# Performance work log

Hardware: AMD Instinct MI355X
Metric: run time of the kernel (lower is better)

## Reference

```python
import jax, jax.numpy as jnp
import numpy as np
import math

B, L, DM = 2, 2048, 1536
H, FD = 12, 16          # num_heads, feature_dim
DV = DM // H            # head_dim = 128
D2 = FD * FD            # expanded Taylor feature dim = 256
CHUNK = 128
EPS = 1e-12
LN_EPS = 1e-5


def setup_inputs() -> dict:
    key = jax.random.key(0)
    ks = jax.random.split(key, 5)
    s = lambda fan_in: 1.0 / math.sqrt(fan_in)
    return {
        "hidden_states": jax.random.normal(ks[0], (B, L, DM), jnp.float32),
        "Wq": jax.random.normal(ks[1], (DM, H * FD), jnp.float32) * s(DM),
        "Wk": jax.random.normal(ks[2], (DM, H * FD), jnp.float32) * s(DM),
        "Wv": jax.random.normal(ks[3], (DM, H * DV), jnp.float32) * s(DM),
        "Wo": jax.random.normal(ks[4], (H * DV, DM), jnp.float32) * s(H * DV),
        "ln_q_g": jnp.ones((H * FD,), jnp.float32),
        "ln_q_b": jnp.zeros((H * FD,), jnp.float32),
        "ln_k_g": jnp.ones((H * FD,), jnp.float32),
        "ln_k_b": jnp.zeros((H * FD,), jnp.float32),
    }


def _layernorm(x, g, b):
    mu = x.mean(-1, keepdims=True)
    var = ((x - mu) ** 2).mean(-1, keepdims=True)
    return (x - mu) * jax.lax.rsqrt(var + LN_EPS) * g + b


def _taylor_exp(x):
    # x: (b, h, l, d) -> flattened outer product / sqrt(d): (b, h, l, d*d)
    x2 = x[..., :, None] * x[..., None, :]
    return x2.reshape(*x.shape[:-1], -1) / math.sqrt(FD)


def _rebased_forward(hidden_states, Wq, Wk, Wv, Wo, ln_q_g, ln_q_b, ln_k_g, ln_k_b):
    b, l, _ = hidden_states.shape
    q = _layernorm(hidden_states @ Wq, ln_q_g, ln_q_b)
    k = _layernorm(hidden_states @ Wk, ln_k_g, ln_k_b)
    v = hidden_states @ Wv
    # (b, l, h*d) -> (b, h, l, d)
    q = q.reshape(b, l, H, FD).transpose(0, 2, 1, 3)
    k = k.reshape(b, l, H, FD).transpose(0, 2, 1, 3)
    v = v.reshape(b, l, H, DV).transpose(0, 2, 1, 3)
    q2 = _taylor_exp(q)  # (b, h, l, D2)
    k2 = _taylor_exp(k)

    nC = l // CHUNK
    # chunk-major layout for scan: (nC, b, h, C, .)
    q2c = q2.reshape(b, H, nC, CHUNK, D2).transpose(2, 0, 1, 3, 4)
    k2c = k2.reshape(b, H, nC, CHUNK, D2).transpose(2, 0, 1, 3, 4)
    vc = v.reshape(b, H, nC, CHUNK, DV).transpose(2, 0, 1, 3, 4)
    mask = jnp.tril(jnp.ones((CHUNK, CHUNK), q2.dtype))  # causal within chunk

    S0 = jnp.zeros((b, H, D2, DV), q2.dtype)  # running sum of k2^T v
    z0 = jnp.zeros((b, H, D2), q2.dtype)      # running sum of k2

    def step(carry, inp):
        S, z = carry
        qc, kc, vcur = inp
        A = jnp.einsum("bhcd,bhed->bhce", qc, kc) * mask  # intra-chunk scores
        num = jnp.einsum("bhcd,bhdv->bhcv", qc, S) + jnp.einsum("bhce,bhev->bhcv", A, vcur)
        den = jnp.einsum("bhcd,bhd->bhc", qc, z) + A.sum(-1)
        o = num / (den[..., None] + EPS)
        S = S + jnp.einsum("bhed,bhev->bhdv", kc, vcur)
        z = z + kc.sum(2)
        return (S, z), o

    _, o = jax.lax.scan(step, (S0, z0), (q2c, k2c, vc))
    # (nC, b, h, C, dv) -> (b, l, h*dv)
    o = o.transpose(1, 2, 0, 3, 4).reshape(b, H, l, DV).transpose(0, 2, 1, 3).reshape(b, l, H * DV)
    return o @ Wo


def reference(hidden_states, Wq, Wk, Wv, Wo, ln_q_g, ln_q_b, ln_k_g, ln_k_b):
    return _rebased_forward(hidden_states, Wq, Wk, Wv, Wo, ln_q_g, ln_q_b, ln_k_g, ln_k_b)
```

## Files before the change

### kernel.cpp

```cpp
#include <hip/hip_runtime.h>
#include <hip/hip_bf16.h>
#include <math.h>

#define Bc   2
#define Lc   2048
#define DMc  1536
#define Hc   12
#define FDc  16
#define DVc  128
#define D2c  256
#define CHK  128
#define NCH  16
#define ROWS (Bc*Lc)
#define HFD  (Hc*FDc)
#define HDV  (Hc*DVc)
#define NQK  (2*HFD)
#define NPRJ (NQK + HDV)

typedef __bf16 bf16x8 __attribute__((ext_vector_type(8)));
typedef float f32x4 __attribute__((ext_vector_type(4)));

__device__ __forceinline__ float bf2f(unsigned short u) {
    return __uint_as_float(((unsigned int)u) << 16);
}
__device__ __forceinline__ unsigned short f2bf(float v) {
    unsigned int u = __float_as_uint(v);
    unsigned int r = (u + 0x7FFFu + ((u >> 16) & 1u)) >> 16;
    return (unsigned short)r;
}
__device__ __forceinline__ unsigned int pack2(unsigned short a, unsigned short b) {
    return (unsigned int)a | ((unsigned int)b << 16);
}
__device__ __forceinline__ float ldin(const void* p, size_t i, int isf32) {
    return isf32 ? ((const float*)p)[i] : bf2f(((const unsigned short*)p)[i]);
}

#define GLL16(g, l) __builtin_amdgcn_global_load_lds( \
    (const __attribute__((address_space(1))) unsigned int*)(g), \
    (__attribute__((address_space(3))) unsigned int*)(l), 16, 0, 0)

__global__ void probe_dtype(const unsigned short* __restrict__ hs, int* __restrict__ flag) {
    const int tid = threadIdx.x;
    int sane = 0;
    for (int i = tid; i < 1024; i += 256) {
        unsigned short b = hs[2 * i];
        int e = (b >> 7) & 0xFF;
        if (e >= 97 && e <= 157) sane++;
    }
    __shared__ int tot;
    if (tid == 0) tot = 0;
    __syncthreads();
    atomicAdd(&tot, sane);
    __syncthreads();
    if (tid == 0) *flag = (tot >= 614) ? 0 : 1;
}

__global__ __launch_bounds__(256) void prep_all(const void* __restrict__ hs,
                                                const void* __restrict__ Wq,
                                                const void* __restrict__ Wk,
                                                const void* __restrict__ Wv,
                                                const void* __restrict__ Wo,
                                                unsigned short* __restrict__ hsb,
                                                unsigned short* __restrict__ Wqkvt,
                                                unsigned short* __restrict__ Wot,
                                                const int* __restrict__ flagp) {
    const int f = *flagp;
    const int t = threadIdx.x;
    int id = blockIdx.x;
    if (id >= 1296) {
        const int n4 = ROWS * DMc / 4;
        int i = (id - 1296) * 256 + t;
        if (i < n4) {
            if (f) {
                float4 x = ((const float4*)hs)[i];
                ushort4 y;
                y.x = f2bf(x.x); y.y = f2bf(x.y); y.z = f2bf(x.z); y.w = f2bf(x.w);
                ((ushort4*)hsb)[i] = y;
            } else {
                ((ushort4*)hsb)[i] = ((const ushort4*)hs)[i];
            }
        }
        return;
    }
    __shared__ float tile[64][65];
    const void* W; unsigned short* Wt; int rows, cols, bx, by;
    if (id < 72)       { W = Wq; Wt = Wqkvt;                          rows = DMc; cols = HFD; bx = (id % 3) * 64;  by = (id / 3) * 64; }
    else if (id < 144) { id -= 72;  W = Wk; Wt = Wqkvt + (size_t)HFD * DMc; rows = DMc; cols = HFD; bx = (id % 3) * 64;  by = (id / 3) * 64; }
    else if (id < 720) { id -= 144; W = Wv; Wt = Wqkvt + (size_t)NQK * DMc; rows = DMc; cols = HDV; bx = (id % 24) * 64; by = (id / 24) * 64; }
    else               { id -= 720; W = Wo; Wt = Wot;                 rows = HDV; cols = DMc; bx = (id % 24) * 64; by = (id / 24) * 64; }
#pragma unroll
    for (int u = 0; u < 16; u++) {
        int idx = t + u * 256;
        int r = idx >> 6, c = idx & 63;
        tile[r][c] = ldin(W, (size_t)(by + r) * cols + bx + c, f);
    }
    __syncthreads();
#pragma unroll
    for (int u = 0; u < 16; u++) {
        int idx = t + u * 256;
        int r = idx >> 6, c = idx & 63;
        Wt[(size_t)(bx + r) * rows + by + c] = f2bf(tile[c][r]);
    }
}

__global__ __launch_bounds__(512) void gemm_mfma_bt(const unsigned short* __restrict__ A,
                                                    const unsigned short* __restrict__ Bt,
                                                    void* __restrict__ C,
                                                    int M, int N, int K,
                                                    int ldc,
                                                    int cMode, const int* __restrict__ flagp,
                                                    unsigned short* __restrict__ vTout) {
    const int f = *flagp;
    __shared__ __align__(16) unsigned char smem[32768];
    unsigned short* As = (unsigned short*)smem;
    unsigned short* Bsu = As + 8192;
    f32x4* scr4 = (f32x4*)smem;

    const int tid = threadIdx.x;
    const int wave = tid >> 6, lane = tid & 63;
    const int kgrp = wave >> 2;
    const int w4 = wave & 3;
    const int lin = blockIdx.y * gridDim.x + blockIdx.x;
    const int nwg = gridDim.x * gridDim.y;
    const int swz = (lin & 7) * (nwg >> 3) + (lin >> 3);
    const int row0 = (swz / gridDim.x) * 128, col0 = (swz % gridDim.x) * 128;
    const int wrow = (w4 >> 1) * 64, wcol = (w4 & 1) * 64;
    const int mlane = lane & 15, quad = lane >> 4;
    const int kHalf = K >> 1;

    const unsigned short* Ab = A + (size_t)row0 * K + (size_t)kgrp * kHalf;
    const unsigned short* Bb = Bt + (size_t)col0 * K + (size_t)kgrp * kHalf;
    const int t256 = tid & 255;
    const int r0 = t256 >> 2;
    const int kc = (t256 & 3) * 8;
    const size_t off0 = (size_t)r0 * K + kc;
    const size_t off1 = (size_t)(r0 + 64) * K + kc;
    char* AsW = (char*)As + kgrp * 8192 + w4 * 1024;
    char* BsW = (char*)Bsu + kgrp * 8192 + w4 * 1024;
    const int ldsBase = kgrp * 4096;

    f32x4 acc[4][4] = {};

    for (int k0 = 0; k0 < kHalf; k0 += 32) {
        GLL16(Ab + off0 + k0, AsW);
        GLL16(Ab + off1 + k0, AsW + 4096);
        GLL16(Bb + off0 + k0, BsW);
        GLL16(Bb + off1 + k0, BsW + 4096);
        __syncthreads();
        bf16x8 a[4], b[4];
#pragma unroll
        for (int i = 0; i < 4; i++)
            a[i] = *(const bf16x8*)&As[ldsBase + (wrow + i * 16 + mlane) * 32 + quad * 8];
#pragma unroll
        for (int j = 0; j < 4; j++)
            b[j] = *(const bf16x8*)&Bsu[ldsBase + (wcol + j * 16 + mlane) * 32 + quad * 8];
#pragma unroll
        for (int i = 0; i < 4; i++)
#pragma unroll
            for (int j = 0; j < 4; j++)
                acc[i][j] = __builtin_amdgcn_mfma_f32_16x16x32_bf16(a[i], b[j], acc[i][j], 0, 0, 0);
        __syncthreads();
    }

    {
        const int col = (wave & 1) * 64 + lane;
        if (kgrp == 1 && w4 < 2) {
#pragma unroll
            for (int i = 0; i < 4; i++)
#pragma unroll
                for (int j = 0; j < 4; j++)
                    scr4[(i * 4 + j) * 128 + col] = acc[i][j];
        }
        __syncthreads();
        if (kgrp == 0 && w4 < 2) {
#pragma unroll
            for (int i = 0; i < 4; i++)
#pragma unroll
                for (int j = 0; j < 4; j++)
                    acc[i][j] += scr4[(i * 4 + j) * 128 + col];
        }
        __syncthreads();
        if (kgrp == 1 && w4 >= 2) {
#pragma unroll
            for (int i = 0; i < 4; i++)
#pragma unroll
                for (int j = 0; j < 4; j++)
                    scr4[(i * 4 + j) * 128 + col] = acc[i][j];
        }
        __syncthreads();
        if (kgrp == 0 && w4 >= 2) {
#pragma unroll
            for (int i = 0; i < 4; i++)
#pragma unroll
                for (int j = 0; j < 4; j++)
                    acc[i][j] += scr4[(i * 4 + j) * 128 + col];
        }
    }
    if (kgrp != 0) return;

    float* Cf = nullptr;
    unsigned short* Cb16 = nullptr;
    bool doT = false;
    int tOff = 0;
    if (cMode == 0) Cf = (float*)C;
    else if (cMode == 1) Cb16 = (unsigned short*)C;
    else if (cMode == 2) { if (f) Cf = (float*)C; else Cb16 = (unsigned short*)C; }
    else if (cMode == 4) {
        if (col0 < NQK) Cf = (float*)C;
        else { doT = true; tOff = NQK; }
    }
    if (cMode <= 3 && vTout) doT = true;

#pragma unroll
    for (int i = 0; i < 4; i++)
#pragma unroll
        for (int j = 0; j < 4; j++) {
            const int col = col0 + wcol + j * 16 + mlane;
            if (Cf) {
#pragma unroll
                for (int r = 0; r < 4; r++) {
                    const int row = row0 + wrow + i * 16 + quad * 4 + r;
                    Cf[(size_t)row * ldc + col] = acc[i][j][r];
                }
            } else if (Cb16) {
#pragma unroll
                for (int r = 0; r < 4; r++) {
                    const int row = row0 + wrow + i * 16 + quad * 4 + r;
                    Cb16[(size_t)row * ldc + col] = f2bf(acc[i][j][r]);
                }
            }
            if (doT) {
                ushort4 pk;
                pk.x = f2bf(acc[i][j][0]); pk.y = f2bf(acc[i][j][1]);
                pk.z = f2bf(acc[i][j][2]); pk.w = f2bf(acc[i][j][3]);
                *(ushort4*)(vTout + (size_t)(col - tOff) * M + row0 + wrow + i * 16 + quad * 4) = pk;
            }
        }
}

__global__ __launch_bounds__(192) void ln_kernel(const float* __restrict__ qk,
                                                 float* __restrict__ q, float* __restrict__ k,
                                                 const void* __restrict__ gq,
                                                 const void* __restrict__ bq,
                                                 const void* __restrict__ gk,
                                                 const void* __restrict__ bk,
                                                 const int* __restrict__ flagp) {
    const int f = *flagp;
    const int row = blockIdx.x, t = threadIdx.x;
    float vq = qk[(size_t)row * NQK + t];
    float vk = qk[(size_t)row * NQK + HFD + t];
    float s[4] = {vq, vq * vq, vk, vk * vk};
    __shared__ float part[4][3];
    const int w = t >> 6, lane = t & 63;
#pragma unroll
    for (int i = 0; i < 4; i++) {
        float v = s[i];
        for (int off = 32; off; off >>= 1) v += __shfl_down(v, off);
        if (lane == 0) part[i][w] = v;
    }
    __syncthreads();
    float sq  = part[0][0] + part[0][1] + part[0][2];
    float sq2 = part[1][0] + part[1][1] + part[1][2];
    float sk  = part[2][0] + part[2][1] + part[2][2];
    float sk2 = part[3][0] + part[3][1] + part[3][2];
    const float inv = 1.0f / (float)HFD;
    float muq = sq * inv, muk = sk * inv;
    float varq = sq2 * inv - muq * muq;
    float vark = sk2 * inv - muk * muk;
    float oq = (vq - muq) * rsqrtf(varq + 1e-5f) * ldin(gq, t, f) + ldin(bq, t, f);
    float ok = (vk - muk) * rsqrtf(vark + 1e-5f) * ldin(gk, t, f) + ldin(bk, t, f);
    q[(size_t)row * HFD + t] = oq;
    k[(size_t)row * HFD + t] = ok;
}

__global__ __launch_bounds__(256) void state_prefix_mfma(const float* __restrict__ kn,
                                                         const unsigned short* __restrict__ vT,
                                                         unsigned short* __restrict__ St,
                                                         float* __restrict__ zc) {
    const int lin = blockIdx.x;
    const int swz = (lin & 7) * 96 + (lin >> 3);
    const int bx = swz & 15;
    const int by = (swz >> 4) & 1;
    const int bh = swz >> 5;
    const int h = bh % Hc, b = bh / Hc;
    const int t0 = bx * 16;
    const int tid = threadIdx.x;
    const int wave = tid >> 6, lane = tid & 63;
    const int mlane = lane & 15, quad = lane >> 4;

    __shared__ __align__(16) float kcs[CHK * FDc];
    __shared__ __align__(16) unsigned short K2t[16 * 136];
    __shared__ __align__(16) unsigned short Vs[64 * 136];
    __shared__ float zp[16][17];
    __shared__ float zpre[16];
    if (tid < 16) zpre[tid] = 0.f;

    f32x4 acc = {};
    const int kr = tid >> 1, khf = tid & 1;
    const int d2l = tid & 15, cg = tid >> 4;
    const int vrow = tid >> 2, vseg = tid & 3;
    const int dvL = wave * 16 + mlane;

    for (int n = 0; n < NCH; n++) {
        const int row0 = b * Lc + n * CHK;
        __syncthreads();
        {
            const float4* src = (const float4*)(kn + (size_t)(row0 + kr) * HFD + h * FDc + khf * 8);
            *(float4*)(kcs + kr * 16 + khf * 8)     = src[0];
            *(float4*)(kcs + kr * 16 + khf * 8 + 4) = src[1];
            const uint4* g = (const uint4*)(vT + (size_t)(h * 128 + by * 64 + vrow) * ROWS + row0 + vseg * 32);
            *(uint4*)(Vs + vrow * 136 + vseg * 32)      = g[0];
            *(uint4*)(Vs + vrow * 136 + vseg * 32 + 8)  = g[1];
            *(uint4*)(Vs + vrow * 136 + vseg * 32 + 16) = g[2];
            *(uint4*)(Vs + vrow * 136 + vseg * 32 + 24) = g[3];
        }
        __syncthreads();
        {
            float zs_ = 0.f;
            unsigned short pk[8];
#pragma unroll
            for (int u = 0; u < 8; u++) {
                int c = cg * 8 + u;
                float p = kcs[c * 16 + bx] * kcs[c * 16 + d2l] * 0.25f;
                zs_ += p;
                pk[u] = f2bf(p);
            }
            uint4 w;
            w.x = pack2(pk[0], pk[1]); w.y = pack2(pk[2], pk[3]);
            w.z = pack2(pk[4], pk[5]); w.w = pack2(pk[6], pk[7]);
            *(uint4*)(K2t + d2l * 136 + cg * 8) = w;
            zp[d2l][cg] = zs_;
        }
        __syncthreads();
        {
            size_t base = (((size_t)(bh * NCH + n) * 16 + bx) * 128) * 16;
            int dv = by * 64 + dvL;
            ushort4 pk;
            pk.x = f2bf(acc[0]); pk.y = f2bf(acc[1]);
            pk.z = f2bf(acc[2]); pk.w = f2bf(acc[3]);
            *(ushort4*)(St + base + (size_t)dv * 16 + quad * 4) = pk;
            if (tid < 16) {
                float s = 0.f;
#pragma unroll
                for (int c = 0; c < 16; c++) s += zp[tid][c];
                if (by == 0)
                    zc[(size_t)(bh * NCH + n) * D2c + t0 + tid] = zpre[tid];
                zpre[tid] += s;
            }
        }
        {
#pragma unroll
            for (int ks = 0; ks < 4; ks++) {
                bf16x8 a = *(const bf16x8*)(K2t + mlane * 136 + ks * 32 + quad * 8);
                bf16x8 bfr = *(const bf16x8*)(Vs + dvL * 136 + ks * 32 + quad * 8);
                acc = __builtin_amdgcn_mfma_f32_16x16x32_bf16(a, bfr, acc, 0, 0, 0);
            }
        }
    }
}

__global__ __launch_bounds__(256) void chunk_out_mfma(const float* __restrict__ qn,
                                                      const float* __restrict__ kn,
                                                      const unsigned short* __restrict__ St,
                                                      const float* __restrict__ z,
                                                      const unsigned short* __restrict__ vT,
                                                      unsigned short* __restrict__ o) {
    const int lin = blockIdx.x;
    const int blk = (lin & 7) * 48 + (lin >> 3);
    const int n = blk & 15, bh = blk >> 4;
    const int h = bh % Hc, b = bh / Hc;
    const int row0 = b * Lc + n * CHK;
    const int tid = threadIdx.x;
    const int wave = tid >> 6, lane = tid & 63;
    const int mlane = lane & 15, quad = lane >> 4;
    const int wrow = (wave >> 1) * 64, wcol = (wave & 1) * 64;

    __shared__ __align__(16) unsigned char lds[61952];
    float* Qs   = (float*)lds;
    float* zs   = (float*)(lds + 8192);
    float* denp = (float*)(lds + 9216);
    float* dinv = (float*)(lds + 10240);
    unsigned char* U = lds + 10752;
    unsigned short* Q2s = (unsigned short*)U;
    unsigned short* Sts = (unsigned short*)(U + 10240);
    unsigned short* Kb  = (unsigned short*)U;
    unsigned short* Qb  = (unsigned short*)(U + 8192);
    unsigned short* At  = (unsigned short*)(U + 16384);
    unsigned short* Vs  = (unsigned short*)U;

    {
        int r = tid >> 1, hf = tid & 1;
        const float4* src = (const float4*)(qn + (size_t)(row0 + r) * HFD + h * FDc + hf * 8);
        *(float4*)(Qs + r * 16 + hf * 8)     = src[0];
        *(float4*)(Qs + r * 16 + hf * 8 + 4) = src[1];
        if (tid < 64)
            ((float4*)zs)[tid] = ((const float4*)(z + ((size_t)bh * NCH + n) * D2c))[tid];
    }
    __syncthreads();

    const int qc = tid >> 1, qhalf = tid & 1;
    float qr[16];
#pragma unroll
    for (int ff = 0; ff < 16; ff++) qr[ff] = Qs[qc * 16 + ff];

    f32x4 acc[4][4] = {};
    float den1 = 0.f;
    const unsigned short* Stb = St + ((size_t)bh * NCH + n) * ((size_t)D2c * DVc);

    for (int k0 = 0; k0 < 256; k0 += 32) {
        {
            unsigned short pk[16];
#pragma unroll
            for (int kk = 0; kk < 16; kk++) {
                int d2 = k0 + qhalf * 16 + kk;
                float val = qr[d2 >> 4] * qr[d2 & 15] * 0.25f;
                den1 += val * zs[d2];
                pk[kk] = f2bf(val);
            }
            uint4 w0, w1;
            w0.x = pack2(pk[0], pk[1]);  w0.y = pack2(pk[2], pk[3]);
            w0.z = pack2(pk[4], pk[5]);  w0.w = pack2(pk[6], pk[7]);
            w1.x = pack2(pk[8], pk[9]);  w1.y = pack2(pk[10], pk[11]);
            w1.z = pack2(pk[12], pk[13]); w1.w = pack2(pk[14], pk[15]);
            *(uint4*)(Q2s + qc * 40 + qhalf * 16) = w0;
            *(uint4*)(Q2s + qc * 40 + qhalf * 16 + 8) = w1;
        }
        {
            int r = tid >> 1, hf = tid & 1;
            const uint4* g = (const uint4*)(Stb + (size_t)((k0 >> 4) + hf) * 2048 + r * 16);
            uint4 d0 = g[0], d1 = g[1];
            *(uint4*)(Sts + r * 40 + hf * 16) = d0;
            *(uint4*)(Sts + r * 40 + hf * 16 + 8) = d1;
        }
        __syncthreads();
        bf16x8 a[4], bfr[4];
#pragma unroll
        for (int i = 0; i < 4; i++)
            a[i] = *(const bf16x8*)(Q2s + (wrow + i * 16 + mlane) * 40 + quad * 8);
#pragma unroll
        for (int j = 0; j < 4; j++)
            bfr[j] = *(const bf16x8*)(Sts + (wcol + j * 16 + mlane) * 40 + quad * 8);
#pragma unroll
        for (int i = 0; i < 4; i++)
#pragma unroll
            for (int j = 0; j < 4; j++)
                acc[i][j] = __builtin_amdgcn_mfma_f32_16x16x32_bf16(a[i], bfr[j], acc[i][j], 0, 0, 0);
        __syncthreads();
    }
    denp[qhalf * 128 + qc] = den1;

    {
        int r = tid >> 1, hf = tid & 1;
        if (hf == 0) {
            unsigned short pq[16], pkk[16];
#pragma unroll
            for (int ff = 0; ff < 16; ff++) pq[ff] = f2bf(Qs[r * 16 + ff]);
            const float* kg = kn + (size_t)(row0 + r) * HFD + h * FDc;
#pragma unroll
            for (int ff = 0; ff < 16; ff++) pkk[ff] = f2bf(kg[ff]);
            uint4 w;
            w.x = pack2(pq[0], pq[1]);  w.y = pack2(pq[2], pq[3]);
            w.z = pack2(pq[4], pq[5]);  w.w = pack2(pq[6], pq[7]);
            *(uint4*)(Qb + r * 32) = w;
            w.x = pack2(pq[8], pq[9]);  w.y = pack2(pq[10], pq[11]);
            w.z = pack2(pq[12], pq[13]); w.w = pack2(pq[14], pq[15]);
            *(uint4*)(Qb + r * 32 + 8) = w;
            w.x = pack2(pkk[0], pkk[1]);  w.y = pack2(pkk[2], pkk[3]);
            w.z = pack2(pkk[4], pkk[5]);  w.w = pack2(pkk[6], pkk[7]);
            *(uint4*)(Kb + r * 32) = w;
            w.x = pack2(pkk[8], pkk[9]);  w.y = pack2(pkk[10], pkk[11]);
            w.z = pack2(pkk[12], pkk[13]); w.w = pack2(pkk[14], pkk[15]);
            *(uint4*)(Kb + r * 32 + 8) = w;
        } else {
            uint4 zz = make_uint4(0, 0, 0, 0);
            *(uint4*)(Qb + r * 32 + 16) = zz;
            *(uint4*)(Qb + r * 32 + 24) = zz;
            *(uint4*)(Kb + r * 32 + 16) = zz;
            *(uint4*)(Kb + r * 32 + 24) = zz;
        }
    }
    __syncthreads();

    {
        f32x4 pacc[4][4] = {};
        bf16x8 a[4], bfr[4];
#pragma unroll
        for (int i = 0; i < 4; i++)
            a[i] = *(const bf16x8*)(Qb + (wrow + i * 16 + mlane) * 32 + quad * 8);
#pragma unroll
        for (int j = 0; j < 4; j++)
            bfr[j] = *(const bf16x8*)(Kb + (wcol + j * 16 + mlane) * 32 + quad * 8);
#pragma unroll
        for (int i = 0; i < 4; i++)
#pragma unroll
            for (int j = 0; j < 4; j++)
                pacc[i][j] = __builtin_amdgcn_mfma_f32_16x16x32_bf16(a[i], bfr[j], pacc[i][j], 0, 0, 0);
#pragma unroll
        for (int i = 0; i < 4; i++)
#pragma unroll
            for (int j = 0; j < 4; j++) {
                int e = wcol + j * 16 + mlane;
#pragma unroll
                for (int r = 0; r < 4; r++) {
                    int c = wrow + i * 16 + quad * 4 + r;
                    float p = pacc[i][j][r];
                    float aval = (e <= c) ? p * p * 0.0625f : 0.f;
                    At[c * 136 + e] = f2bf(aval);
                }
            }
    }
    __syncthreads();

    if (tid < 128) {
        float rs = 0.f;
#pragma unroll
        for (int e8 = 0; e8 < 128; e8 += 8) {
            bf16x8 v8 = *(const bf16x8*)(At + tid * 136 + e8);
#pragma unroll
            for (int u = 0; u < 8; u++) rs += (float)v8[u];
        }
        dinv[tid] = 1.0f / (denp[tid] + denp[128 + tid] + rs + 1e-12f);
    }

    for (int e0 = 0; e0 < 128; e0 += 32) {
        {
            int r = tid >> 1, hf = tid & 1;
            const uint4* g = (const uint4*)(vT + (size_t)(h * 128 + r) * ROWS + row0 + e0 + hf * 16);
            uint4 d0 = g[0], d1 = g[1];
            *(uint4*)(Vs + r * 40 + hf * 16) = d0;
            *(uint4*)(Vs + r * 40 + hf * 16 + 8) = d1;
        }
        __syncthreads();
        bf16x8 a[4], bfr[4];
#pragma unroll
        for (int i = 0; i < 4; i++)
            a[i] = *(const bf16x8*)(At + (wrow + i * 16 + mlane) * 136 + e0 + quad * 8);
#pragma unroll
        for (int j = 0; j < 4; j++)
            bfr[j] = *(const bf16x8*)(Vs + (wcol + j * 16 + mlane) * 40 + quad * 8);
#pragma unroll
        for (int i = 0; i < 4; i++)
#pragma unroll
            for (int j = 0; j < 4; j++)
                acc[i][j] = __builtin_amdgcn_mfma_f32_16x16x32_bf16(a[i], bfr[j], acc[i][j], 0, 0, 0);
        __syncthreads();
    }

#pragma unroll
    for (int i = 0; i < 4; i++)
#pragma unroll
        for (int j = 0; j < 4; j++) {
            int col = h * 128 + wcol + j * 16 + mlane;
#pragma unroll
            for (int r = 0; r < 4; r++) {
                int c = wrow + i * 16 + quad * 4 + r;
                o[(size_t)(row0 + c) * HDV + col] = f2bf(acc[i][j][r] * dinv[c]);
            }
        }
}

extern "C" void kernel_launch(void* const* d_in, const int* in_sizes, int n_in,
                              void* d_out, int out_size, void* d_ws, size_t ws_size,
                              hipStream_t stream) {
    const void* hs = d_in[0];
    const void* Wq = d_in[1];
    const void* Wk = d_in[2];
    const void* Wv = d_in[3];
    const void* Wo = d_in[4];
    const void* gq = d_in[5];
    const void* bq = d_in[6];
    const void* gk = d_in[7];
    const void* bk = d_in[8];

    int* flag = (int*)d_ws;
    float* base = (float*)d_ws + 16;
    float* qpre = base;
    float* kpre = qpre + (size_t)ROWS * HFD;
    float* vreg = kpre + (size_t)ROWS * HFD;
    float* Sc   = vreg + (size_t)ROWS * HDV;
    float* zc   = Sc + (size_t)Bc * Hc * NCH * D2c * DVc;
    float* fend = zc + (size_t)Bc * Hc * NCH * D2c;
    unsigned short* hsb = (unsigned short*)fend;
    unsigned short* ob  = hsb;
    unsigned short* Wot = hsb + (size_t)ROWS * DMc;
    unsigned short* vT  = Wot + (size_t)HDV * DMc;
    float* qk = Sc;
    unsigned short* Wqkvt = (unsigned short*)(Sc + (size_t)ROWS * NQK);
    unsigned short* St = (unsigned short*)vreg;

    probe_dtype<<<1, 256, 0, stream>>>((const unsigned short*)hs, flag);

    prep_all<<<1296 + ROWS * DMc / 1024, 256, 0, stream>>>(
        hs, Wq, Wk, Wv, Wo, hsb, Wqkvt, Wot, flag);

    gemm_mfma_bt<<<dim3(NPRJ / 128, ROWS / 128), 512, 0, stream>>>(
        hsb, Wqkvt, qk, ROWS, NPRJ, DMc, NQK, 4, flag, vT);

    ln_kernel<<<ROWS, HFD, 0, stream>>>(qk, qpre, kpre, gq, bq, gk, bk, flag);

    state_prefix_mfma<<<16 * 2 * Bc * Hc, 256, 0, stream>>>(kpre, vT, St, zc);

    chunk_out_mfma<<<Bc * Hc * NCH, 256, 0, stream>>>(qpre, kpre, St, zc, vT, ob);

    gemm_mfma_bt<<<dim3(DMc / 128, ROWS / 128), 512, 0, stream>>>(
        ob, Wot, d_out, ROWS, DMc, HDV, DMc, 2, flag, nullptr);
}
```

Before: 235.5 us.

## Split chunk_out reduction dimension across two wave groups with LDS reduction

```diff
diff --git a/kernel.cpp b/kernel.cpp
--- a/kernel.cpp
+++ b/kernel.cpp
@@ -359,7 +359,7 @@
     }
 }
 
-__global__ __launch_bounds__(256) void chunk_out_mfma(const float* __restrict__ qn,
+__global__ __launch_bounds__(512) void chunk_out_mfma(const float* __restrict__ qn,
                                                       const float* __restrict__ kn,
                                                       const unsigned short* __restrict__ St,
                                                       const float* __restrict__ z,
@@ -372,42 +372,71 @@
     const int row0 = b * Lc + n * CHK;
     const int tid = threadIdx.x;
     const int wave = tid >> 6, lane = tid & 63;
+    const int kgrp = wave >> 2, w4 = wave & 3;
+    const int t256 = tid & 255;
     const int mlane = lane & 15, quad = lane >> 4;
-    const int wrow = (wave >> 1) * 64, wcol = (wave & 1) * 64;
-
-    __shared__ __align__(16) unsigned char lds[61952];
-    float* Qs   = (float*)lds;
-    float* zs   = (float*)(lds + 8192);
-    float* denp = (float*)(lds + 9216);
-    float* dinv = (float*)(lds + 10240);
-    unsigned char* U = lds + 10752;
-    unsigned short* Q2s = (unsigned short*)U;
-    unsigned short* Sts = (unsigned short*)(U + 10240);
-    unsigned short* Kb  = (unsigned short*)U;
-    unsigned short* Qb  = (unsigned short*)(U + 8192);
-    unsigned short* At  = (unsigned short*)(U + 16384);
-    unsigned short* Vs  = (unsigned short*)U;
+    const int wrow = (w4 >> 1) * 64, wcol = (w4 & 1) * 64;
+
+    __shared__ __align__(16) unsigned char lds[60928];
+    float* zs   = (float*)lds;
+    float* denp = (float*)(lds + 1024);
+    float* dinv = (float*)(lds + 3072);
+    unsigned short* Qb  = (unsigned short*)(lds + 3584);
+    unsigned short* Kb  = (unsigned short*)(lds + 11776);
+    float* Qs   = (float*)(lds + 19968);
+    unsigned short* Q2s = (unsigned short*)(lds + 19968);
+    unsigned short* Sts = (unsigned short*)(lds + 40448);
+    unsigned short* At  = (unsigned short*)(lds + 22016);
+    unsigned short* Vs1 = (unsigned short*)(lds + 3584);
+    f32x4* scr4 = (f32x4*)(lds + 3584);
 
     {
-        int r = tid >> 1, hf = tid & 1;
-        const float4* src = (const float4*)(qn + (size_t)(row0 + r) * HFD + h * FDc + hf * 8);
-        *(float4*)(Qs + r * 16 + hf * 8)     = src[0];
-        *(float4*)(Qs + r * 16 + hf * 8 + 4) = src[1];
+        int r = tid >> 2, q4 = tid & 3;
+        const float4* src = (const float4*)(qn + (size_t)(row0 + r) * HFD + h * FDc + q4 * 4);
+        *(float4*)(Qs + r * 16 + q4 * 4) = src[0];
         if (tid < 64)
             ((float4*)zs)[tid] = ((const float4*)(z + ((size_t)bh * NCH + n) * D2c))[tid];
     }
     __syncthreads();
 
-    const int qc = tid >> 1, qhalf = tid & 1;
+    const int qc = t256 >> 1, qhalf = t256 & 1;
     float qr[16];
 #pragma unroll
     for (int ff = 0; ff < 16; ff++) qr[ff] = Qs[qc * 16 + ff];
+
+    {
+        int r = tid >> 2, q4 = tid & 3;
+        uint4 zz = make_uint4(0, 0, 0, 0);
+        unsigned short p8[8];
+        if (q4 < 2) {
+#pragma unroll
+            for (int ff = 0; ff < 8; ff++) p8[ff] = f2bf(Qs[r * 16 + q4 * 8 + ff]);
+            uint4 w;
+            w.x = pack2(p8[0], p8[1]); w.y = pack2(p8[2], p8[3]);
+            w.z = pack2(p8[4], p8[5]); w.w = pack2(p8[6], p8[7]);
+            *(uint4*)(Qb + r * 32 + q4 * 8) = w;
+            *(uint4*)(Qb + r * 32 + 16 + q4 * 8) = zz;
+        } else {
+            const float* kg = kn + (size_t)(row0 + r) * HFD + h * FDc + (q4 - 2) * 8;
+#pragma unroll
+            for (int ff = 0; ff < 8; ff++) p8[ff] = f2bf(kg[ff]);
+            uint4 w;
+            w.x = pack2(p8[0], p8[1]); w.y = pack2(p8[2], p8[3]);
+            w.z = pack2(p8[4], p8[5]); w.w = pack2(p8[6], p8[7]);
+            *(uint4*)(Kb + r * 32 + (q4 - 2) * 8) = w;
+            *(uint4*)(Kb + r * 32 + 16 + (q4 - 2) * 8) = zz;
+        }
+    }
+    __syncthreads();
 
     f32x4 acc[4][4] = {};
     float den1 = 0.f;
     const unsigned short* Stb = St + ((size_t)bh * NCH + n) * ((size_t)D2c * DVc);
-
-    for (int k0 = 0; k0 < 256; k0 += 32) {
+    unsigned short* Q2g = Q2s + kgrp * (128 * 40);
+    unsigned short* Stg = Sts + kgrp * (128 * 40);
+
+    for (int s = 0; s < 4; s++) {
+        const int k0 = kgrp * 128 + s * 32;
         {
             unsigned short pk[16];
 #pragma unroll
@@ -422,24 +451,23 @@
             w0.z = pack2(pk[4], pk[5]);  w0.w = pack2(pk[6], pk[7]);
             w1.x = pack2(pk[8], pk[9]);  w1.y = pack2(pk[10], pk[11]);
             w1.z = pack2(pk[12], pk[13]); w1.w = pack2(pk[14], pk[15]);
-            *(uint4*)(Q2s + qc * 40 + qhalf * 16) = w0;
-            *(uint4*)(Q2s + qc * 40 + qhalf * 16 + 8) = w1;
+            *(uint4*)(Q2g + qc * 40 + qhalf * 16) = w0;
+            *(uint4*)(Q2g + qc * 40 + qhalf * 16 + 8) = w1;
         }
         {
-            int r = tid >> 1, hf = tid & 1;
-            const uint4* g = (const uint4*)(Stb + (size_t)((k0 >> 4) + hf) * 2048 + r * 16);
+            const uint4* g = (const uint4*)(Stb + (size_t)((k0 >> 4) + qhalf) * 2048 + qc * 16);
             uint4 d0 = g[0], d1 = g[1];
-            *(uint4*)(Sts + r * 40 + hf * 16) = d0;
-            *(uint4*)(Sts + r * 40 + hf * 16 + 8) = d1;
+            *(uint4*)(Stg + qc * 40 + qhalf * 16) = d0;
+            *(uint4*)(Stg + qc * 40 + qhalf * 16 + 8) = d1;
         }
         __syncthreads();
         bf16x8 a[4], bfr[4];
 #pragma unroll
         for (int i = 0; i < 4; i++)
-            a[i] = *(const bf16x8*)(Q2s + (wrow + i * 16 + mlane) * 40 + quad * 8);
+            a[i] = *(const bf16x8*)(Q2g + (wrow + i * 16 + mlane) * 40 + quad * 8);
 #pragma unroll
         for (int j = 0; j < 4; j++)
-            bfr[j] = *(const bf16x8*)(Sts + (wcol + j * 16 + mlane) * 40 + quad * 8);
+            bfr[j] = *(const bf16x8*)(Stg + (wcol + j * 16 + mlane) * 40 + quad * 8);
 #pragma unroll
         for (int i = 0; i < 4; i++)
 #pragma unroll
@@ -447,62 +475,31 @@
                 acc[i][j] = __builtin_amdgcn_mfma_f32_16x16x32_bf16(a[i], bfr[j], acc[i][j], 0, 0, 0);
         __syncthreads();
     }
-    denp[qhalf * 128 + qc] = den1;
+    denp[(kgrp * 2 + qhalf) * 128 + qc] = den1;
 
     {
-        int r = tid >> 1, hf = tid & 1;
-        if (hf == 0) {
-            unsigned short pq[16], pkk[16];
-#pragma unroll
-            for (int ff = 0; ff < 16; ff++) pq[ff] = f2bf(Qs[r * 16 + ff]);
-            const float* kg = kn + (size_t)(row0 + r) * HFD + h * FDc;
-#pragma unroll
-            for (int ff = 0; ff < 16; ff++) pkk[ff] = f2bf(kg[ff]);
-            uint4 w;
-            w.x = pack2(pq[0], pq[1]);  w.y = pack2(pq[2], pq[3]);
-            w.z = pack2(pq[4], pq[5]);  w.w = pack2(pq[6], pq[7]);
-            *(uint4*)(Qb + r * 32) = w;
-            w.x = pack2(pq[8], pq[9]);  w.y = pack2(pq[10], pq[11]);
-            w.z = pack2(pq[12], pq[13]); w.w = pack2(pq[14], pq[15]);
-            *(uint4*)(Qb + r * 32 + 8) = w;
-            w.x = pack2(pkk[0], pkk[1]);  w.y = pack2(pkk[2], pkk[3]);
-            w.z = pack2(pkk[4], pkk[5]);  w.w = pack2(pkk[6], pkk[7]);
-            *(uint4*)(Kb + r * 32) = w;
-            w.x = pack2(pkk[8], pkk[9]);  w.y = pack2(pkk[10], pkk[11]);
-            w.z = pack2(pkk[12], pkk[13]); w.w = pack2(pkk[14], pkk[15]);
-            *(uint4*)(Kb + r * 32 + 8) = w;
-        } else {
-            uint4 zz = make_uint4(0, 0, 0, 0);
-            *(uint4*)(Qb + r * 32 + 16) = zz;
-            *(uint4*)(Qb + r * 32 + 24) = zz;
-            *(uint4*)(Kb + r * 32 + 16) = zz;
-            *(uint4*)(Kb + r * 32 + 24) = zz;
-        }
-    }
-    __syncthreads();
-
-    {
-        f32x4 pacc[4][4] = {};
-        bf16x8 a[4], bfr[4];
-#pragma unroll
-        for (int i = 0; i < 4; i++)
-            a[i] = *(const bf16x8*)(Qb + (wrow + i * 16 + mlane) * 32 + quad * 8);
-#pragma unroll
-        for (int j = 0; j < 4; j++)
-            bfr[j] = *(const bf16x8*)(Kb + (wcol + j * 16 + mlane) * 32 + quad * 8);
-#pragma unroll
-        for (int i = 0; i < 4; i++)
-#pragma unroll
-            for (int j = 0; j < 4; j++)
+        const int rowblk = wave >> 2, colblk = wave & 3;
+        f32x4 pacc[4][2] = {};
+        bf16x8 a[4], bfr[2];
+#pragma unroll
+        for (int i = 0; i < 4; i++)
+            a[i] = *(const bf16x8*)(Qb + (rowblk * 64 + i * 16 + mlane) * 32 + quad * 8);
+#pragma unroll
+        for (int j = 0; j < 2; j++)
+            bfr[j] = *(const bf16x8*)(Kb + (colblk * 32 + j * 16 + mlane) * 32 + quad * 8);
+#pragma unroll
+        for (int i = 0; i < 4; i++)
+#pragma unroll
+            for (int j = 0; j < 2; j++)
                 pacc[i][j] = __builtin_amdgcn_mfma_f32_16x16x32_bf16(a[i], bfr[j], pacc[i][j], 0, 0, 0);
 #pragma unroll
         for (int i = 0; i < 4; i++)
 #pragma unroll
-            for (int j = 0; j < 4; j++) {
-                int e = wcol + j * 16 + mlane;
+            for (int j = 0; j < 2; j++) {
+                int e = colblk * 32 + j * 16 + mlane;
 #pragma unroll
                 for (int r = 0; r < 4; r++) {
-                    int c = wrow + i * 16 + quad * 4 + r;
+                    int c = rowblk * 64 + i * 16 + quad * 4 + r;
                     float p = pacc[i][j][r];
                     float aval = (e <= c) ? p * p * 0.0625f : 0.f;
                     At[c * 136 + e] = f2bf(aval);
@@ -519,16 +516,16 @@
 #pragma unroll
             for (int u = 0; u < 8; u++) rs += (float)v8[u];
         }
-        dinv[tid] = 1.0f / (denp[tid] + denp[128 + tid] + rs + 1e-12f);
-    }
-
-    for (int e0 = 0; e0 < 128; e0 += 32) {
+        dinv[tid] = 1.0f / (denp[tid] + denp[128 + tid] + denp[256 + tid] + denp[384 + tid] + rs + 1e-12f);
+    }
+
+    for (int s2 = 0; s2 < 2; s2++) {
+        const int e0 = kgrp * 64 + s2 * 32;
         {
-            int r = tid >> 1, hf = tid & 1;
-            const uint4* g = (const uint4*)(vT + (size_t)(h * 128 + r) * ROWS + row0 + e0 + hf * 16);
+            const uint4* g = (const uint4*)(vT + (size_t)(h * 128 + qc) * ROWS + row0 + e0 + qhalf * 16);
             uint4 d0 = g[0], d1 = g[1];
-            *(uint4*)(Vs + r * 40 + hf * 16) = d0;
-            *(uint4*)(Vs + r * 40 + hf * 16 + 8) = d1;
+            *(uint4*)(Vs1 + qc * 72 + kgrp * 32 + qhalf * 16) = d0;
+            *(uint4*)(Vs1 + qc * 72 + kgrp * 32 + qhalf * 16 + 8) = d1;
         }
         __syncthreads();
         bf16x8 a[4], bfr[4];
@@ -537,7 +534,7 @@
             a[i] = *(const bf16x8*)(At + (wrow + i * 16 + mlane) * 136 + e0 + quad * 8);
 #pragma unroll
         for (int j = 0; j < 4; j++)
-            bfr[j] = *(const bf16x8*)(Vs + (wcol + j * 16 + mlane) * 40 + quad * 8);
+            bfr[j] = *(const bf16x8*)(Vs1 + (wcol + j * 16 + mlane) * 72 + kgrp * 32 + quad * 8);
 #pragma unroll
         for (int i = 0; i < 4; i++)
 #pragma unroll
@@ -545,6 +542,42 @@
                 acc[i][j] = __builtin_amdgcn_mfma_f32_16x16x32_bf16(a[i], bfr[j], acc[i][j], 0, 0, 0);
         __syncthreads();
     }
+
+    {
+        const int col = (w4 & 1) * 64 + lane;
+        if (kgrp == 1 && w4 < 2) {
+#pragma unroll
+            for (int i = 0; i < 4; i++)
+#pragma unroll
+                for (int j = 0; j < 4; j++)
+                    scr4[(i * 4 + j) * 128 + col] = acc[i][j];
+        }
+        __syncthreads();
+        if (kgrp == 0 && w4 < 2) {
+#pragma unroll
+            for (int i = 0; i < 4; i++)
+#pragma unroll
+                for (int j = 0; j < 4; j++)
+                    acc[i][j] += scr4[(i * 4 + j) * 128 + col];
+        }
+        __syncthreads();
+        if (kgrp == 1 && w4 >= 2) {
+#pragma unroll
+            for (int i = 0; i < 4; i++)
+#pragma unroll
+                for (int j = 0; j < 4; j++)
+                    scr4[(i * 4 + j) * 128 + col] = acc[i][j];
+        }
+        __syncthreads();
+        if (kgrp == 0 && w4 >= 2) {
+#pragma unroll
+            for (int i = 0; i < 4; i++)
+#pragma unroll
+                for (int j = 0; j < 4; j++)
+                    acc[i][j] += scr4[(i * 4 + j) * 128 + col];
+        }
+    }
+    if (kgrp != 0) return;
 
 #pragma unroll
     for (int i = 0; i < 4; i++)
@@ -600,7 +633,7 @@
 
     state_prefix_mfma<<<16 * 2 * Bc * Hc, 256, 0, stream>>>(kpre, vT, St, zc);
 
-    chunk_out_mfma<<<Bc * Hc * NCH, 256, 0, stream>>>(qpre, kpre, St, zc, vT, ob);
+    chunk_out_mfma<<<Bc * Hc * NCH, 512, 0, stream>>>(qpre, kpre, St, zc, vT, ob);
 
     gemm_mfma_bt<<<dim3(DMc / 128, ROWS / 128), 512, 0, stream>>>(
         ob, Wot, d_out, ROWS, DMc, HDV, DMc, 2, flag, nullptr);
```

Result: slower. 246.1 us, median of 2 (+4.5%).
